# Kernel optimization log

Measured on AMD Instinct MI355X. Metric: run time of the kernel, lower is better.

The kernel has to match this reference:

```python
import jax, jax.numpy as jnp
import numpy as np

N_HEADS = 16
WINDOW = 256
GLOBAL_IDX = np.array([0])

def _global_local_mask(seq_len):
    # allowed[i,j] = True if |i-j|<=window OR i is global OR j is global
    i = jnp.arange(seq_len)[:, None]
    j = jnp.arange(seq_len)[None, :]
    g = jnp.asarray(GLOBAL_IDX)
    row_global = jnp.isin(jnp.arange(seq_len), g)
    allowed = (jnp.abs(i - j) <= WINDOW) | row_global[:, None] | row_global[None, :]
    return allowed

def setup_inputs() -> dict:
    key = jax.random.key(0)
    ks = jax.random.split(key, 9)
    B, S, D = 1, 2048, 1024
    w = 0.02
    return {
        "x": jax.random.normal(ks[0], (B, S, D), jnp.float32),
        "Wq": jax.random.normal(ks[1], (D, D), jnp.float32) * w,
        "bq": jnp.zeros((D,), jnp.float32),
        "Wk": jax.random.normal(ks[2], (D, D), jnp.float32) * w,
        "bk": jnp.zeros((D,), jnp.float32),
        "Wv": jax.random.normal(ks[3], (D, D), jnp.float32) * w,
        "bv": jnp.zeros((D,), jnp.float32),
        "Wo": jax.random.normal(ks[4], (D, D), jnp.float32) * w,
        "bo": jnp.zeros((D,), jnp.float32),
    }

def reference(x, Wq, bq, Wk, bk, Wv, bv, Wo, bo):
    B, S, D = x.shape
    H = N_HEADS
    Dh = D // H
    scale = Dh ** -0.5
    # projections (torch Linear: y = x @ W^T + b; here W stored as [in,out] equivalent)
    q = (x @ Wq + bq).reshape(B, S, H, Dh)
    k = (x @ Wk + bk).reshape(B, S, H, Dh)
    v = (x @ Wv + bv).reshape(B, S, H, Dh)
    # dense scores [B,H,S,S]
    scores = jnp.einsum("bqhd,bkhd->bhqk", q, k) * scale
    allowed = _global_local_mask(S)  # [S,S] bool
    scores = jnp.where(allowed[None, None], scores, -jnp.inf)
    attn = jax.nn.softmax(scores, axis=-1)
    out = jnp.einsum("bhqk,bkhd->bqhd", attn, v).reshape(B, S, D)
    return out @ Wo + bo
```

## Files before the change

### kernel.cpp

```cpp
#include <hip/hip_runtime.h>
#include <hip/hip_bf16.h>
#include <math.h>

#define S_LEN   2048
#define DM      1024
#define NH      16
#define DH      64
#define WIN     256

typedef __attribute__((ext_vector_type(8))) short          bf16x8;
typedef __attribute__((ext_vector_type(4))) float          f32x4;
typedef __attribute__((ext_vector_type(8))) unsigned short u16x8;
typedef __attribute__((ext_vector_type(4))) unsigned short u16x4;
typedef unsigned short u16;

#define GLDS(gsrc, ldst)                                                        \
    __builtin_amdgcn_global_load_lds(                                           \
        (const __attribute__((address_space(1))) void*)(gsrc),                  \
        (__attribute__((address_space(3))) void*)(ldst), 16, 0, 0)

__device__ __forceinline__ u16 f2bf(float f) {
    union { float f; unsigned u; } v; v.f = f;
    unsigned r = v.u + 0x7FFF + ((v.u >> 16) & 1);
    return (u16)(r >> 16);
}

__global__ __launch_bounds__(256) void cvt_x_kernel(const float* __restrict__ x,
                                                    u16* __restrict__ xb) {
    int i = (blockIdx.x * 256 + threadIdx.x) * 8;
    float4 a = *(const float4*)&x[i];
    float4 b = *(const float4*)&x[i + 4];
    u16x8 o;
    o[0] = f2bf(a.x); o[1] = f2bf(a.y); o[2] = f2bf(a.z); o[3] = f2bf(a.w);
    o[4] = f2bf(b.x); o[5] = f2bf(b.y); o[6] = f2bf(b.z); o[7] = f2bf(b.w);
    *(u16x8*)&xb[i] = o;
}

__global__ __launch_bounds__(256) void cvt_wT_kernel(const float* __restrict__ Wq,
                                                     const float* __restrict__ Wk,
                                                     const float* __restrict__ Wv,
                                                     const float* __restrict__ Wo,
                                                     u16* __restrict__ WT) {
    __shared__ float Ws[64][65];
    const float* W = (blockIdx.z == 0) ? Wq : (blockIdx.z == 1) ? Wk
                   : (blockIdx.z == 2) ? Wv : Wo;
    u16* dst = WT + (size_t)blockIdx.z * (1u << 20);
    const int k0 = blockIdx.x * 64, n0 = blockIdx.y * 64;
    const int tid = threadIdx.x;
#pragma unroll
    for (int p = 0; p < 4; ++p) {
        int flat = tid + p * 256;
        int row = flat >> 4, c4 = (flat & 15) * 4;
        float4 v = *(const float4*)&W[(k0 + row) * DM + n0 + c4];
        Ws[row][c4 + 0] = v.x; Ws[row][c4 + 1] = v.y;
        Ws[row][c4 + 2] = v.z; Ws[row][c4 + 3] = v.w;
    }
    __syncthreads();
#pragma unroll
    for (int p = 0; p < 4; ++p) {
        int flat = tid + p * 256;
        int n = flat >> 4, k4 = (flat & 15) * 4;
        u16x4 o;
#pragma unroll
        for (int j = 0; j < 4; ++j) o[j] = f2bf(Ws[k4 + j][n]);
        *(u16x4*)&dst[(n0 + n) * DM + k0 + k4] = o;
    }
}

template<int OMODE>
__device__ __forceinline__ void gemm_mfma_body(const u16* __restrict__ A,
                                               const u16* __restrict__ Bt,
                                               const float* __restrict__ bias,
                                               u16* __restrict__ Cb,
                                               float* __restrict__ Cf) {
    __shared__ __align__(16) u16 As[64 * 64];
    __shared__ __align__(16) u16 Bs[128 * 64];
    const int tid = threadIdx.x;
    const int l = tid & 63, w = tid >> 6;
    const int wm = w >> 1, wn = w & 1;
    const int l15 = l & 15, lh = l >> 4;
    const int brow = blockIdx.y * 64, bcol = blockIdx.x * 128;

    f32x4 acc[2][4];
#pragma unroll
    for (int i = 0; i < 2; ++i)
#pragma unroll
        for (int j = 0; j < 4; ++j) acc[i][j] = (f32x4)0.f;

    const int lr = l >> 3, lc = l & 7, g = lc ^ lr;
    const u16* aSrc = A  + (size_t)(brow + w * 16 + lr) * DM + g * 8;
    const u16* bSrc = Bt + (size_t)(bcol + w * 32 + lr) * DM + g * 8;

    for (int k0 = 0; k0 < DM; k0 += 64) {
        __syncthreads();
#pragma unroll
        for (int i = 0; i < 2; ++i)
            GLDS(aSrc + i * 8 * DM + k0, &As[(w * 2 + i) * 512]);
#pragma unroll
        for (int i = 0; i < 4; ++i)
            GLDS(bSrc + i * 8 * DM + k0, &Bs[(w * 4 + i) * 512]);
        __syncthreads();

#pragma unroll
        for (int ks = 0; ks < 2; ++ks) {
            bf16x8 af[2], bf[4];
#pragma unroll
            for (int i = 0; i < 2; ++i) {
                int ra = wm * 32 + i * 16 + l15;
                af[i] = *(const bf16x8*)&As[ra * 64 + (((ks * 4 + lh) ^ (ra & 7)) * 8)];
            }
#pragma unroll
            for (int j = 0; j < 4; ++j) {
                int rb = wn * 64 + j * 16 + l15;
                bf[j] = *(const bf16x8*)&Bs[rb * 64 + (((ks * 4 + lh) ^ (rb & 7)) * 8)];
            }
#pragma unroll
            for (int i = 0; i < 2; ++i)
#pragma unroll
                for (int j = 0; j < 4; ++j)
                    acc[i][j] = __builtin_amdgcn_mfma_f32_16x16x32_bf16(af[i], bf[j], acc[i][j], 0, 0, 0);
        }
    }
#pragma unroll
    for (int j = 0; j < 4; ++j) {
        int gcol = bcol + wn * 64 + j * 16 + l15;
        float bz = bias[gcol];
#pragma unroll
        for (int i = 0; i < 2; ++i) {
            int grow = brow + wm * 32 + i * 16 + lh * 4;
            if (OMODE == 2) {
                u16x4 tv;
#pragma unroll
                for (int rr = 0; rr < 4; ++rr) tv[rr] = f2bf(acc[i][j][rr] + bz);
                *(u16x4*)&Cb[(size_t)gcol * S_LEN + grow] = tv;
            } else {
#pragma unroll
                for (int rr = 0; rr < 4; ++rr) {
                    float v = acc[i][j][rr] + bz;
                    if (OMODE == 0) Cb[(grow + rr) * DM + gcol] = f2bf(v);
                    else            Cf[(grow + rr) * DM + gcol] = v;
                }
            }
        }
    }
}

__global__ __launch_bounds__(256) void qkv_mfma_kernel(
        const u16* __restrict__ xb,
        const u16* __restrict__ WqT, const float* __restrict__ bq, u16* __restrict__ Qb,
        const u16* __restrict__ WkT, const float* __restrict__ bk, u16* __restrict__ Kb,
        const u16* __restrict__ WvT, const float* __restrict__ bv, u16* __restrict__ VT) {
    if (blockIdx.z == 0)      gemm_mfma_body<0>(xb, WqT, bq, Qb, nullptr);
    else if (blockIdx.z == 1) gemm_mfma_body<0>(xb, WkT, bk, Kb, nullptr);
    else                      gemm_mfma_body<2>(xb, WvT, bv, VT, nullptr);
}

__global__ __launch_bounds__(256) void oproj_mfma_kernel(
        const u16* __restrict__ Ob, const u16* __restrict__ WoT,
        const float* __restrict__ bo, float* __restrict__ out) {
    gemm_mfma_body<1>(Ob, WoT, bo, nullptr, out);
}

__global__ __launch_bounds__(256, 4) void attn_mfma_kernel(
        const u16* __restrict__ Qb, const u16* __restrict__ Kb,
        const u16* __restrict__ VT, u16* __restrict__ Ob) {
    __shared__ __align__(16) u16 Pl[4 * 16 * 72];
    __shared__ __align__(16) float MB[2][64][20];
    const int tid = threadIdx.x;
    const int w = tid >> 6, l = tid & 63;
    const int qg = w >> 1, half = w & 1;
    const int l15 = l & 15, lh = l >> 4;
    const int i0 = blockIdx.x * 32, h = blockIdx.y;
    const int q0 = i0 + qg * 16;
    u16* Pw = &Pl[w * 16 * 72];

    bf16x8 qf[2];
    {
        int qr = q0 + l15;
        qf[0] = *(const bf16x8*)&Qb[qr * DM + h * DH + lh * 8];
        qf[1] = *(const bf16x8*)&Qb[qr * DM + h * DH + 32 + lh * 8];
    }

    f32x4 o[4];
    float ls[4] = {0.f, 0.f, 0.f, 0.f};
#pragma unroll
    for (int fc = 0; fc < 4; ++fc) o[fc] = (f32x4)0.f;

    int t_lo, t_hi;
    {
        int lo = q0 - WIN;      if (lo < 0) lo = 0;
        int hi = q0 + 15 + WIN; if (hi > S_LEN - 1) hi = S_LEN - 1;
        if (q0 == 0) hi = S_LEN - 1;
        t_lo = lo >> 6; t_hi = hi >> 6;
    }
    const int nband = t_hi - t_lo + 1;
    const int nt = nband + (t_lo > 0 ? 1 : 0);
    const int b0 = half ? ((nt + 1) >> 1) : 0;
    const int b1 = half ? nt : ((nt + 1) >> 1);

    bf16x8 kf[2][4];
    if (b0 < b1) {
        const int j0 = ((b0 < nband) ? (t_lo + b0) : 0) << 6;
#pragma unroll
        for (int ks = 0; ks < 2; ++ks)
#pragma unroll
            for (int fc = 0; fc < 4; ++fc)
                kf[ks][fc] = *(const bf16x8*)&Kb[(j0 + fc * 16 + l15) * DM + h * DH + ks * 32 + lh * 8];
    }

    for (int it = b0; it < b1; ++it) {
        const int j0 = ((it < nband) ? (t_lo + it) : 0) << 6;

        bf16x8 vf[2][4];
#pragma unroll
        for (int ks = 0; ks < 2; ++ks)
#pragma unroll
            for (int fc = 0; fc < 4; ++fc)
                vf[ks][fc] = *(const bf16x8*)&VT[(h * DH + fc * 16 + l15) * S_LEN + j0 + ks * 32 + lh * 8];

        f32x4 s[4];
#pragma unroll
        for (int fc = 0; fc < 4; ++fc) s[fc] = (f32x4)0.f;
#pragma unroll
        for (int ks = 0; ks < 2; ++ks)
#pragma unroll
            for (int fc = 0; fc < 4; ++fc)
                s[fc] = __builtin_amdgcn_mfma_f32_16x16x32_bf16(qf[ks], kf[ks][fc], s[fc], 0, 0, 0);

        const int itn = (it + 1 < b1) ? it + 1 : it;
        const int jn = ((itn < nband) ? (t_lo + itn) : 0) << 6;
        bf16x8 kn[2][4];
#pragma unroll
        for (int ks = 0; ks < 2; ++ks)
#pragma unroll
            for (int fc = 0; fc < 4; ++fc)
                kn[ks][fc] = *(const bf16x8*)&Kb[(jn + fc * 16 + l15) * DM + h * DH + ks * 32 + lh * 8];

#pragma unroll
        for (int fc = 0; fc < 4; ++fc)
#pragma unroll
            for (int rr = 0; rr < 4; ++rr) {
                int r = q0 + lh * 4 + rr;
                int c = j0 + fc * 16 + l15;
                int d = r - c;
                bool ok = (d <= WIN && -d <= WIN) || (r == 0) || (c == 0);
                s[fc][rr] = ok ? __expf(s[fc][rr] * 0.125f) : 0.f;
            }
#pragma unroll
        for (int rr = 0; rr < 4; ++rr)
            ls[rr] += (s[0][rr] + s[1][rr]) + (s[2][rr] + s[3][rr]);

#pragma unroll
        for (int fc = 0; fc < 4; ++fc)
#pragma unroll
            for (int rr = 0; rr < 4; ++rr)
                Pw[(lh * 4 + rr) * 72 + fc * 16 + l15] = f2bf(s[fc][rr]);
        asm volatile("s_waitcnt lgkmcnt(0)" ::: "memory");

#pragma unroll
        for (int ks = 0; ks < 2; ++ks) {
            bf16x8 pa = *(const bf16x8*)&Pw[l15 * 72 + ks * 32 + lh * 8];
#pragma unroll
            for (int fc = 0; fc < 4; ++fc)
                o[fc] = __builtin_amdgcn_mfma_f32_16x16x32_bf16(pa, vf[ks][fc], o[fc], 0, 0, 0);
        }

#pragma unroll
        for (int ks = 0; ks < 2; ++ks)
#pragma unroll
            for (int fc = 0; fc < 4; ++fc)
                kf[ks][fc] = kn[ks][fc];
    }

    if (half == 1) {
#pragma unroll
        for (int fc = 0; fc < 4; ++fc)
            *(f32x4*)&MB[qg][l][fc * 4] = o[fc];
        *(f32x4*)&MB[qg][l][16] = (f32x4){ls[0], ls[1], ls[2], ls[3]};
    }
    __syncthreads();
    if (half == 0) {
#pragma unroll
        for (int fc = 0; fc < 4; ++fc) {
            f32x4 po = *(const f32x4*)&MB[qg][l][fc * 4];
            o[fc] += po;
        }
        f32x4 pl = *(const f32x4*)&MB[qg][l][16];
#pragma unroll
        for (int rr = 0; rr < 4; ++rr) ls[rr] += pl[rr];

#pragma unroll
        for (int rr = 0; rr < 4; ++rr)
#pragma unroll
            for (int mk = 1; mk < 16; mk <<= 1)
                ls[rr] += __shfl_xor(ls[rr], mk, 64);

#pragma unroll
        for (int rr = 0; rr < 4; ++rr) {
            float inv = 1.0f / ls[rr];
#pragma unroll
            for (int fc = 0; fc < 4; ++fc)
                Ob[(q0 + lh * 4 + rr) * DM + h * DH + fc * 16 + l15] = f2bf(o[fc][rr] * inv);
        }
    }
}

extern "C" void kernel_launch(void* const* d_in, const int* in_sizes, int n_in,
                              void* d_out, int out_size, void* d_ws, size_t ws_size,
                              hipStream_t stream) {
    const float* x  = (const float*)d_in[0];
    const float* Wq = (const float*)d_in[1];
    const float* bq = (const float*)d_in[2];
    const float* Wk = (const float*)d_in[3];
    const float* bk = (const float*)d_in[4];
    const float* Wv = (const float*)d_in[5];
    const float* bv = (const float*)d_in[6];
    const float* Wo = (const float*)d_in[7];
    const float* bo = (const float*)d_in[8];
    float* out = (float*)d_out;

    char* W = (char*)d_ws;
    u16* xb  = (u16*)(W);
    u16* WT  = (u16*)(W + ((size_t)4  << 20));
    u16* Qb  = (u16*)(W + ((size_t)12 << 20));
    u16* Kb  = (u16*)(W + ((size_t)16 << 20));
    u16* VT  = (u16*)(W + ((size_t)20 << 20));
    u16* Ob  = xb;
    const u16* WqT = WT;
    const u16* WkT = WT + (1u << 20);
    const u16* WvT = WT + (2u << 20);
    const u16* WoT = WT + (3u << 20);

    cvt_x_kernel <<<dim3(S_LEN * DM / (256 * 8)), 256, 0, stream>>>(x, xb);
    cvt_wT_kernel<<<dim3(16, 16, 4), 256, 0, stream>>>(Wq, Wk, Wv, Wo, WT);
    qkv_mfma_kernel<<<dim3(8, 32, 3), 256, 0, stream>>>(xb, WqT, bq, Qb,
                                                        WkT, bk, Kb, WvT, bv, VT);
    attn_mfma_kernel<<<dim3(64, 16), 256, 0, stream>>>(Qb, Kb, VT, Ob);
    oproj_mfma_kernel<<<dim3(8, 32), 256, 0, stream>>>(Ob, WoT, bo, out);
}
```

Before: 198.3 us.

## Share double-buffered K/V tiles in LDS across four query waves

The attention kernel now gives each block 64 query rows, one 16-row group per wave. Each K/V tile is loaded once into swizzled, double-buffered LDS with global_load_lds, and all four waves read from it. Before, each wave loaded K and V straight from global memory and split the key range in half with a cross-wave merge. The aim is to cut redundant global K/V traffic and overlap the next tile's load with compute. A swizzled 1D grid is added for locality, and waves skip tiles outside their own window. The cost is a block barrier on every iteration, a bigger LDS footprint, and some extra tiles per block because the band is the union over 64 rows.

```diff
diff --git a/kernel.cpp b/kernel.cpp
--- a/kernel.cpp
+++ b/kernel.cpp
@@ -161,17 +161,19 @@
     gemm_mfma_body<1>(Ob, WoT, bo, nullptr, out);
 }
 
-__global__ __launch_bounds__(256, 4) void attn_mfma_kernel(
+__global__ __launch_bounds__(256) void attn_mfma_kernel(
         const u16* __restrict__ Qb, const u16* __restrict__ Kb,
         const u16* __restrict__ VT, u16* __restrict__ Ob) {
+    __shared__ __align__(16) u16 Ks[2][64 * 64];
+    __shared__ __align__(16) u16 Vs[2][64 * 64];
     __shared__ __align__(16) u16 Pl[4 * 16 * 72];
-    __shared__ __align__(16) float MB[2][64][20];
     const int tid = threadIdx.x;
     const int w = tid >> 6, l = tid & 63;
-    const int qg = w >> 1, half = w & 1;
     const int l15 = l & 15, lh = l >> 4;
-    const int i0 = blockIdx.x * 32, h = blockIdx.y;
-    const int q0 = i0 + qg * 16;
+
+    const int swz = (blockIdx.x & 7) * 64 + (blockIdx.x >> 3);
+    const int h = swz >> 5, i0 = (swz & 31) * 64;
+    const int q0 = i0 + w * 16;
     u16* Pw = &Pl[w * 16 * 72];
 
     bf16x8 qf[2];
@@ -188,120 +190,115 @@
 
     int t_lo, t_hi;
     {
-        int lo = q0 - WIN;      if (lo < 0) lo = 0;
-        int hi = q0 + 15 + WIN; if (hi > S_LEN - 1) hi = S_LEN - 1;
-        if (q0 == 0) hi = S_LEN - 1;
+        int lo = i0 - WIN;      if (lo < 0) lo = 0;
+        int hi = i0 + 63 + WIN; if (hi > S_LEN - 1) hi = S_LEN - 1;
+        if (i0 == 0) hi = S_LEN - 1;
         t_lo = lo >> 6; t_hi = hi >> 6;
     }
     const int nband = t_hi - t_lo + 1;
     const int nt = nband + (t_lo > 0 ? 1 : 0);
-    const int b0 = half ? ((nt + 1) >> 1) : 0;
-    const int b1 = half ? nt : ((nt + 1) >> 1);
-
-    bf16x8 kf[2][4];
-    if (b0 < b1) {
-        const int j0 = ((b0 < nband) ? (t_lo + b0) : 0) << 6;
-#pragma unroll
-        for (int ks = 0; ks < 2; ++ks)
+    int wt_hi;
+    {
+        int whi = q0 + 15 + WIN; if (whi > S_LEN - 1) whi = S_LEN - 1;
+        wt_hi = whi >> 6;
+    }
+    const bool isglob = (q0 == 0);
+
+    const int lr = l >> 3, g = (l & 7) ^ lr;
+
+    int cur = 0;
+    {
+        const int j0 = t_lo << 6;
+#pragma unroll
+        for (int c2 = 0; c2 < 2; ++c2) {
+            int c = w * 2 + c2;
+            GLDS(&Kb[(size_t)(j0 + c * 8 + lr) * DM + h * DH + g * 8], &Ks[0][c * 512]);
+            GLDS(&VT[(size_t)(h * DH + c * 8 + lr) * S_LEN + j0 + g * 8], &Vs[0][c * 512]);
+        }
+    }
+    __syncthreads();
+
+    for (int it = 0; it < nt; ++it) {
+        const int t = (it < nband) ? (t_lo + it) : 0;
+        const int j0 = t << 6;
+
+        if (it + 1 < nt) {
+            const int jn = ((it + 1 < nband) ? (t_lo + it + 1) : 0) << 6;
+            u16* KsB = Ks[cur ^ 1];
+            u16* VsB = Vs[cur ^ 1];
+#pragma unroll
+            for (int c2 = 0; c2 < 2; ++c2) {
+                int c = w * 2 + c2;
+                GLDS(&Kb[(size_t)(jn + c * 8 + lr) * DM + h * DH + g * 8], &KsB[c * 512]);
+                GLDS(&VT[(size_t)(h * DH + c * 8 + lr) * S_LEN + jn + g * 8], &VsB[c * 512]);
+            }
+        }
+
+        if (isglob || it >= nband || t <= wt_hi) {
+            const u16* Kc = Ks[cur];
+            const u16* Vc = Vs[cur];
+
+            f32x4 s[4];
+#pragma unroll
+            for (int fc = 0; fc < 4; ++fc) s[fc] = (f32x4)0.f;
+#pragma unroll
+            for (int ks = 0; ks < 2; ++ks)
+#pragma unroll
+                for (int fc = 0; fc < 4; ++fc) {
+                    int rb = fc * 16 + l15;
+                    bf16x8 kf = *(const bf16x8*)&Kc[rb * 64 + (((ks * 4 + lh) ^ (rb & 7)) * 8)];
+                    s[fc] = __builtin_amdgcn_mfma_f32_16x16x32_bf16(qf[ks], kf, s[fc], 0, 0, 0);
+                }
+
 #pragma unroll
             for (int fc = 0; fc < 4; ++fc)
-                kf[ks][fc] = *(const bf16x8*)&Kb[(j0 + fc * 16 + l15) * DM + h * DH + ks * 32 + lh * 8];
-    }
-
-    for (int it = b0; it < b1; ++it) {
-        const int j0 = ((it < nband) ? (t_lo + it) : 0) << 6;
-
-        bf16x8 vf[2][4];
-#pragma unroll
-        for (int ks = 0; ks < 2; ++ks)
+#pragma unroll
+                for (int rr = 0; rr < 4; ++rr) {
+                    int r = q0 + lh * 4 + rr;
+                    int c = j0 + fc * 16 + l15;
+                    int d = r - c;
+                    bool ok = (d <= WIN && -d <= WIN) || (r == 0) || (c == 0);
+                    s[fc][rr] = ok ? __expf(s[fc][rr] * 0.125f) : 0.f;
+                }
+#pragma unroll
+            for (int rr = 0; rr < 4; ++rr)
+                ls[rr] += (s[0][rr] + s[1][rr]) + (s[2][rr] + s[3][rr]);
+
 #pragma unroll
             for (int fc = 0; fc < 4; ++fc)
-                vf[ks][fc] = *(const bf16x8*)&VT[(h * DH + fc * 16 + l15) * S_LEN + j0 + ks * 32 + lh * 8];
-
-        f32x4 s[4];
-#pragma unroll
-        for (int fc = 0; fc < 4; ++fc) s[fc] = (f32x4)0.f;
-#pragma unroll
-        for (int ks = 0; ks < 2; ++ks)
-#pragma unroll
-            for (int fc = 0; fc < 4; ++fc)
-                s[fc] = __builtin_amdgcn_mfma_f32_16x16x32_bf16(qf[ks], kf[ks][fc], s[fc], 0, 0, 0);
-
-        const int itn = (it + 1 < b1) ? it + 1 : it;
-        const int jn = ((itn < nband) ? (t_lo + itn) : 0) << 6;
-        bf16x8 kn[2][4];
-#pragma unroll
-        for (int ks = 0; ks < 2; ++ks)
-#pragma unroll
-            for (int fc = 0; fc < 4; ++fc)
-                kn[ks][fc] = *(const bf16x8*)&Kb[(jn + fc * 16 + l15) * DM + h * DH + ks * 32 + lh * 8];
-
+#pragma unroll
+                for (int rr = 0; rr < 4; ++rr)
+                    Pw[(lh * 4 + rr) * 72 + fc * 16 + l15] = f2bf(s[fc][rr]);
+            asm volatile("s_waitcnt lgkmcnt(0)" ::: "memory");
+
+#pragma unroll
+            for (int ks = 0; ks < 2; ++ks) {
+                bf16x8 pa = *(const bf16x8*)&Pw[l15 * 72 + ks * 32 + lh * 8];
+#pragma unroll
+                for (int fc = 0; fc < 4; ++fc) {
+                    int rb = fc * 16 + l15;
+                    bf16x8 vfr = *(const bf16x8*)&Vc[rb * 64 + (((ks * 4 + lh) ^ (rb & 7)) * 8)];
+                    o[fc] = __builtin_amdgcn_mfma_f32_16x16x32_bf16(pa, vfr, o[fc], 0, 0, 0);
+                }
+            }
+        }
+
+        __syncthreads();
+        cur ^= 1;
+    }
+
+#pragma unroll
+    for (int rr = 0; rr < 4; ++rr)
+#pragma unroll
+        for (int mk = 1; mk < 16; mk <<= 1)
+            ls[rr] += __shfl_xor(ls[rr], mk, 64);
+
+#pragma unroll
+    for (int rr = 0; rr < 4; ++rr) {
+        float inv = 1.0f / ls[rr];
 #pragma unroll
         for (int fc = 0; fc < 4; ++fc)
-#pragma unroll
-            for (int rr = 0; rr < 4; ++rr) {
-                int r = q0 + lh * 4 + rr;
-                int c = j0 + fc * 16 + l15;
-                int d = r - c;
-                bool ok = (d <= WIN && -d <= WIN) || (r == 0) || (c == 0);
-                s[fc][rr] = ok ? __expf(s[fc][rr] * 0.125f) : 0.f;
-            }
-#pragma unroll
-        for (int rr = 0; rr < 4; ++rr)
-            ls[rr] += (s[0][rr] + s[1][rr]) + (s[2][rr] + s[3][rr]);
-
-#pragma unroll
-        for (int fc = 0; fc < 4; ++fc)
-#pragma unroll
-            for (int rr = 0; rr < 4; ++rr)
-                Pw[(lh * 4 + rr) * 72 + fc * 16 + l15] = f2bf(s[fc][rr]);
-        asm volatile("s_waitcnt lgkmcnt(0)" ::: "memory");
-
-#pragma unroll
-        for (int ks = 0; ks < 2; ++ks) {
-            bf16x8 pa = *(const bf16x8*)&Pw[l15 * 72 + ks * 32 + lh * 8];
-#pragma unroll
-            for (int fc = 0; fc < 4; ++fc)
-                o[fc] = __builtin_amdgcn_mfma_f32_16x16x32_bf16(pa, vf[ks][fc], o[fc], 0, 0, 0);
-        }
-
-#pragma unroll
-        for (int ks = 0; ks < 2; ++ks)
-#pragma unroll
-            for (int fc = 0; fc < 4; ++fc)
-                kf[ks][fc] = kn[ks][fc];
-    }
-
-    if (half == 1) {
-#pragma unroll
-        for (int fc = 0; fc < 4; ++fc)
-            *(f32x4*)&MB[qg][l][fc * 4] = o[fc];
-        *(f32x4*)&MB[qg][l][16] = (f32x4){ls[0], ls[1], ls[2], ls[3]};
-    }
-    __syncthreads();
-    if (half == 0) {
-#pragma unroll
-        for (int fc = 0; fc < 4; ++fc) {
-            f32x4 po = *(const f32x4*)&MB[qg][l][fc * 4];
-            o[fc] += po;
-        }
-        f32x4 pl = *(const f32x4*)&MB[qg][l][16];
-#pragma unroll
-        for (int rr = 0; rr < 4; ++rr) ls[rr] += pl[rr];
-
-#pragma unroll
-        for (int rr = 0; rr < 4; ++rr)
-#pragma unroll
-            for (int mk = 1; mk < 16; mk <<= 1)
-                ls[rr] += __shfl_xor(ls[rr], mk, 64);
-
-#pragma unroll
-        for (int rr = 0; rr < 4; ++rr) {
-            float inv = 1.0f / ls[rr];
-#pragma unroll
-            for (int fc = 0; fc < 4; ++fc)
-                Ob[(q0 + lh * 4 + rr) * DM + h * DH + fc * 16 + l15] = f2bf(o[fc][rr] * inv);
-        }
+            Ob[(q0 + lh * 4 + rr) * DM + h * DH + fc * 16 + l15] = f2bf(o[fc][rr] * inv);
     }
 }
 
@@ -335,6 +332,6 @@
     cvt_wT_kernel<<<dim3(16, 16, 4), 256, 0, stream>>>(Wq, Wk, Wv, Wo, WT);
     qkv_mfma_kernel<<<dim3(8, 32, 3), 256, 0, stream>>>(xb, WqT, bq, Qb,
                                                         WkT, bk, Kb, WvT, bv, VT);
-    attn_mfma_kernel<<<dim3(64, 16), 256, 0, stream>>>(Qb, Kb, VT, Ob);
+    attn_mfma_kernel<<<dim3(512), 256, 0, stream>>>(Qb, Kb, VT, Ob);
     oproj_mfma_kernel<<<dim3(8, 32), 256, 0, stream>>>(Ob, WoT, bo, out);
 }
```

Measured after the change: 168.8 us. 1.17x faster.
